# Kernel tuning notes

Measured on AMD Instinct MI355X. Metric: run time of the kernel, lower is better.

The kernel has to match this reference:

```python
import jax, jax.numpy as jnp
import numpy as np

# Grid derived from defaults: pc_range=(0,-40,-3,70.4,40,1), voxel=(0.2,0.2,4)
GX, GY = 352, 400          # round((70.4-0)/0.2), round((40-(-40))/0.2)
B, P = 4, 65536            # samples, points per sample
NSEG = B * GX * GY + 1     # dense pillar-id space + 1 sentinel for masked points
OUT_CH = 64
BN_EPS = 1e-3


def setup_inputs() -> dict:
    key = jax.random.key(0)
    k1, k2, k3 = jax.random.split(key, 3)
    xyz_min = jnp.array([0.0, -40.0, -3.0], jnp.float32)
    xyz_max = jnp.array([70.4, 40.0, 1.0], jnp.float32)
    xyz = jax.random.uniform(k1, (B, P, 3), jnp.float32, minval=xyz_min, maxval=xyz_max)
    rest = jax.random.normal(k2, (B, P, 4), jnp.float32)  # rcs, v_r, v_r_comp, time
    points = jnp.concatenate([xyz, rest], axis=-1)        # [B, P, 7]
    W = jax.random.normal(k3, (OUT_CH, 13), jnp.float32) * (1.0 / np.sqrt(13.0))
    gamma = jnp.ones((OUT_CH,), jnp.float32)
    beta = jnp.zeros((OUT_CH,), jnp.float32)
    return {"points": points, "W": W, "gamma": gamma, "beta": beta}


def reference(points, W, gamma, beta):
    Bn, Pn, _ = points.shape
    pts = points.reshape(Bn * Pn, 7)                      # [N, 7] (= torch points[:, 1:])
    dtype = pts.dtype
    voxel = jnp.array([0.2, 0.2, 4.0], dtype)
    pc_min = jnp.array([0.0, -40.0, -3.0], dtype)
    batch_idx = jnp.repeat(jnp.arange(Bn, dtype=jnp.int32), Pn)

    coords_f = (pts[:, :3] - pc_min) / voxel              # float voxel coords
    mask = ((coords_f[:, 0] >= 0) & (coords_f[:, 0] < GX)
            & (coords_f[:, 1] >= 0) & (coords_f[:, 1] < GY))
    coords = coords_f.astype(jnp.int32)                   # [N, 3] (cx, cy, cz)
    sentinel = Bn * GX * GY                               # trash segment for masked points
    lin = jnp.where(mask,
                    batch_idx * (GX * GY) + coords[:, 0] * GY + coords[:, 1],
                    sentinel)
    # torch.unique(..., return_inverse=True, dim=0) on (batch, cx, cy) rows ==
    # unique of the bijective linear id (same sorted order).
    unq, unq_inv = jnp.unique(lin, return_inverse=True, size=NSEG, fill_value=sentinel)

    cnt = jax.ops.segment_sum(jnp.ones((lin.shape[0], 1), dtype), unq_inv, num_segments=NSEG)
    mean_xyz = jax.ops.segment_sum(pts[:, :3], unq_inv, num_segments=NSEG) / jnp.maximum(cnt, 1.0)
    f_cluster = pts[:, :3] - mean_xyz[unq_inv]
    f_center = pts[:, :3] - (coords.astype(dtype) * voxel + voxel * 0.5 + pc_min)
    feats = jnp.concatenate([pts, f_cluster, f_center], axis=-1)   # [N, 13]

    # PFN layer (last_layer=True): Linear -> BN1d (training stats) -> ReLU
    x = feats @ W.T                                       # [N, 64]
    mu = x.mean(axis=0)
    var = x.var(axis=0)                                   # biased, as BN training
    x = jax.nn.relu((x - mu) * jax.lax.rsqrt(var + BN_EPS) * gamma + beta)

    fmax = jax.ops.segment_max(x, unq_inv, num_segments=NSEG)     # scatter_max
    x_max = fmax[unq_inv]                                 # gather back (PFN output)
    feat_max = jax.ops.segment_max(x_max, unq_inv, num_segments=NSEG)

    valid = (unq < sentinel)[:, None]                     # real pillars only
    feat_max = jnp.where(valid, feat_max, 0.0)            # padded/empty -> 0

    b = unq // (GX * GY)
    rem = unq % (GX * GY)
    cx = rem // GY
    cy = rem % GY
    coords_out = jnp.stack([b, cy, cx], axis=1).astype(jnp.int32)  # (batch, y, x)
    grid_size = jnp.array([GY, GX], jnp.int32)
    return feat_max, coords_out, grid_size
```

## Files before the change

### kernel.cpp

```cpp
#include <hip/hip_runtime.h>
#include <stdint.h>
#include <utility>

#define NPTS   262144
#define GXGY   140800
#define GYv    400
#define NSEG   563201
#define SENT   563200
#define NB_SCAN 275
#define PIL_BLOCKS 2048
#define MOMG_BLOCKS 512

constexpr size_t alignup(size_t x) { return (x + 255) & ~(size_t)255; }
constexpr size_t O_CNT  = 0;
constexpr size_t O_MOM  = alignup(O_CNT + (size_t)NSEG * 4);
constexpr size_t ZERO_BYTES = alignup(O_MOM + 104 * 4);
constexpr size_t O_PPTR = ZERO_BYTES;
constexpr size_t O_ROWI = alignup(O_PPTR + (size_t)NSEG * 4);
constexpr size_t O_FEAT = alignup(O_ROWI + (size_t)NPTS * 16);
constexpr size_t O_MEAN = alignup(O_FEAT + (size_t)NPTS * 32);
constexpr size_t O_BSO  = alignup(O_MEAN + (size_t)NPTS * 12);
constexpr size_t O_BSC  = alignup(O_BSO + NB_SCAN * 4);
constexpr size_t O_KP   = alignup(O_BSC + NB_SCAN * 4);
constexpr size_t O_WF   = alignup(O_KP + 256);
constexpr size_t O_SH   = alignup(O_WF + 832 * 4);

__device__ __forceinline__ int point_lin(float x, float y, int b, bool& mask) {
  float cxf = x / 0.2f;
  float cyf = (y + 40.0f) / 0.2f;
  int cx = (int)cxf, cy = (int)cyf;
  mask = (cxf >= 0.0f) && (cxf < 352.0f) && (cyf >= 0.0f) && (cyf < 400.0f);
  return mask ? (b * GXGY + cx * GYv + cy) : SENT;
}

__global__ __launch_bounds__(256) void k_count(const float* __restrict__ pts,
                                               unsigned int* __restrict__ cnt) {
  int i = blockIdx.x * 256 + threadIdx.x;
  if (i >= NPTS) return;
  const float* p = pts + (size_t)i * 7;
  float x = p[0], y = p[1];
  bool m;
  int lin = point_lin(x, y, i >> 16, m);
  atomicAdd(&cnt[lin], 1u);
}

__global__ __launch_bounds__(256) void k_scan1(const unsigned int* __restrict__ cnt,
                                               unsigned int* __restrict__ bso,
                                               unsigned int* __restrict__ bsc) {
  int t = threadIdx.x;
  int base = blockIdx.x * 2048 + t * 8;
  const uint4* c4 = (const uint4*)(cnt + base);
  uint4 a = c4[0], b = c4[1];
  unsigned so = (a.x > 0) + (a.y > 0) + (a.z > 0) + (a.w > 0) +
                (b.x > 0) + (b.y > 0) + (b.z > 0) + (b.w > 0);
  unsigned sc = a.x + a.y + a.z + a.w + b.x + b.y + b.z + b.w;
  for (int m = 1; m < 64; m <<= 1) { so += __shfl_xor(so, m); sc += __shfl_xor(sc, m); }
  __shared__ unsigned wo[4], wc[4];
  if ((t & 63) == 0) { wo[t >> 6] = so; wc[t >> 6] = sc; }
  __syncthreads();
  if (t == 0) {
    bso[blockIdx.x] = wo[0] + wo[1] + wo[2] + wo[3];
    bsc[blockIdx.x] = wc[0] + wc[1] + wc[2] + wc[3];
  }
}

__global__ __launch_bounds__(256) void k_scan3(const unsigned int* __restrict__ cnt,
                                               const unsigned int* __restrict__ bso,
                                               const unsigned int* __restrict__ bsc,
                                               uint4* __restrict__ rowinfo,
                                               unsigned int* __restrict__ pptr,
                                               unsigned int* __restrict__ kp) {
  int t = threadIdx.x;
  unsigned vo_m = 0, vc_m = 0, vo_a = 0;
  for (int e = t; e < NB_SCAN; e += 256) {
    unsigned o = bso[e], c = bsc[e];
    vo_a += o;
    if (e < (int)blockIdx.x) { vo_m += o; vc_m += c; }
  }
  for (int m = 1; m < 64; m <<= 1) {
    vo_m += __shfl_xor(vo_m, m);
    vc_m += __shfl_xor(vc_m, m);
    vo_a += __shfl_xor(vo_a, m);
  }
  __shared__ unsigned s0[4], s1[4], s2[4];
  int wv = t >> 6;
  if ((t & 63) == 0) { s0[wv] = vo_m; s1[wv] = vc_m; s2[wv] = vo_a; }
  __syncthreads();
  unsigned boo = s0[0] + s0[1] + s0[2] + s0[3];
  unsigned boc = s1[0] + s1[1] + s1[2] + s1[3];
  unsigned tot = s2[0] + s2[1] + s2[2] + s2[3];
  if (blockIdx.x == 0 && t == 0) *kp = tot;

  int base = blockIdx.x * 2048 + t * 8;
  const uint4* q = (const uint4*)(cnt + base);
  uint4 a = q[0], b = q[1];
  unsigned c[8] = {a.x, a.y, a.z, a.w, b.x, b.y, b.z, b.w};
  unsigned po[8], pc[8];
  unsigned so = 0, sc = 0;
#pragma unroll
  for (int k = 0; k < 8; k++) {
    po[k] = so; pc[k] = sc;
    so += (c[k] > 0); sc += c[k];
  }
  __shared__ unsigned sdo[256], sdc[256];
  __syncthreads();
  sdo[t] = so; sdc[t] = sc;
  __syncthreads();
  for (int off = 1; off < 256; off <<= 1) {
    unsigned ao = (t >= off) ? sdo[t - off] : 0u;
    unsigned ac = (t >= off) ? sdc[t - off] : 0u;
    __syncthreads();
    sdo[t] += ao; sdc[t] += ac;
    __syncthreads();
  }
  unsigned eo = sdo[t] - so + boo;
  unsigned ec = sdc[t] - sc + boc;
#pragma unroll
  for (int k = 0; k < 8; k++) {
    if (c[k] > 0) {
      unsigned r = eo + po[k];
      unsigned start = ec + pc[k];
      rowinfo[r] = make_uint4((unsigned)(base + k), start, c[k], 0u);
      pptr[base + k] = start;
    }
  }
}

__global__ __launch_bounds__(256) void k_sortfeat(const float* __restrict__ pts,
                                                  unsigned int* __restrict__ pptr,
                                                  float* __restrict__ feat) {
  int i = blockIdx.x * 256 + threadIdx.x;
  if (i >= NPTS) return;
  const float* p = pts + (size_t)i * 7;
  float x = p[0], y = p[1], z = p[2];
  bool m;
  int lin = point_lin(x, y, i >> 16, m);
  if (lin == SENT) return;
  unsigned pos = atomicAdd(&pptr[lin], 1u);
  float4* fb = (float4*)(feat + (size_t)pos * 8);
  fb[0] = make_float4(x, y, z, p[3]);
  fb[1] = make_float4(p[4], p[5], p[6], 0.0f);
}

constexpr int tri_j(int t) { int j = 0; while (t >= 13 - j) { t -= 13 - j; j++; } return j; }
constexpr int tri_k(int t) { int j = 0; while (t >= 13 - j) { t -= 13 - j; j++; } return j + t; }

template<int G, size_t U>
__device__ __forceinline__ void accum_one(const float (&f)[13], float (&acc)[52]) {
  constexpr int E = G * 52 + (int)U;
  if constexpr (E < 13) {
    acc[U] += f[E];
  } else {
    constexpr int J = tri_j(E - 13);
    constexpr int K = tri_k(E - 13);
    acc[U] += f[J] * f[K];
  }
}
template<int G, size_t... Us>
__device__ __forceinline__ void accum_all(const float (&f)[13], float (&acc)[52],
                                          std::index_sequence<Us...>) {
  (accum_one<G, Us>(f, acc), ...);
}

template<int G>
__device__ __forceinline__ void momrank_body(const uint4* __restrict__ rowinfo,
                                             const float* __restrict__ feat,
                                             float* __restrict__ meanr,
                                             float* __restrict__ mom,
                                             unsigned kp) {
  float acc[52];
#pragma unroll
  for (int u = 0; u < 52; u++) acc[u] = 0.f;
  const unsigned stride = MOMG_BLOCKS * 256;
  for (unsigned r = (blockIdx.x >> 1) * 256 + threadIdx.x; r < kp; r += stride) {
    uint4 ri = rowinfo[r];
    unsigned start = ri.y, n = ri.z;
    const float4* fp = (const float4*)(feat + (size_t)start * 8);
    float sx = 0.f, sy = 0.f, sz = 0.f;
    for (unsigned p = 0; p < n; p++) { float4 A = fp[2 * p]; sx += A.x; sy += A.y; sz += A.z; }
    float inv = 1.0f / fmaxf((float)n, 1.0f);
    float mx = sx * inv, my = sy * inv, mz = sz * inv;
    if (G == 0) {
      meanr[(size_t)r * 3 + 0] = mx;
      meanr[(size_t)r * 3 + 1] = my;
      meanr[(size_t)r * 3 + 2] = mz;
    }
    for (unsigned p = 0; p < n; p++) {
      float4 A = fp[2 * p], Bq = fp[2 * p + 1];
      float x = A.x, y = A.y, z = A.z;
      int cx = (int)(x / 0.2f);
      int cy = (int)((y + 40.0f) / 0.2f);
      int cz = (int)((z + 3.0f) / 4.0f);
      float f[13] = {x, y, z, A.w, Bq.x, Bq.y, Bq.z,
                     x - mx, y - my, z - mz,
                     x - ((float)cx * 0.2f + 0.1f + 0.0f),
                     y - ((float)cy * 0.2f + 0.1f - 40.0f),
                     z - ((float)cz * 4.0f + 2.0f - 3.0f)};
      accum_all<G>(f, acc, std::make_index_sequence<52>{});
    }
  }
  __shared__ float red[4][52];
  int wv = threadIdx.x >> 6, lane = threadIdx.x & 63;
#pragma unroll
  for (int u = 0; u < 52; u++) {
    float v = acc[u];
    v += __shfl_xor(v, 1);  v += __shfl_xor(v, 2);  v += __shfl_xor(v, 4);
    v += __shfl_xor(v, 8);  v += __shfl_xor(v, 16); v += __shfl_xor(v, 32);
    if (lane == 0) red[wv][u] = v;
  }
  __syncthreads();
  if (threadIdx.x < 52) {
    int u = threadIdx.x;
    atomicAdd(&mom[G * 52 + u], red[0][u] + red[1][u] + red[2][u] + red[3][u]);
  }
}

__global__ __launch_bounds__(256, 2) void k_momrank(const uint4* __restrict__ rowinfo,
                                                    const float* __restrict__ feat,
                                                    float* __restrict__ meanr,
                                                    float* __restrict__ mom,
                                                    const unsigned int* __restrict__ kpp) {
  unsigned kp = *kpp;
  if ((blockIdx.x & 1) == 0) momrank_body<0>(rowinfo, feat, meanr, mom, kp);
  else                       momrank_body<1>(rowinfo, feat, meanr, mom, kp);
}

__global__ void k_bnfinal(const float* __restrict__ W,
                          const float* __restrict__ g,
                          const float* __restrict__ bta,
                          const float* __restrict__ mom,
                          float* __restrict__ wf,
                          float* __restrict__ sh) {
  int c = threadIdx.x;
  float w[13];
#pragma unroll
  for (int j = 0; j < 13; j++) w[j] = W[c * 13 + j];
  const float invN = 1.0f / (float)NPTS;
  float mu = 0.f;
#pragma unroll
  for (int j = 0; j < 13; j++) mu += w[j] * (mom[j] * invN);
  float e2 = 0.f;
  int mi = 13;
#pragma unroll
  for (int j = 0; j < 13; j++) {
#pragma unroll
    for (int k = j; k < 13; k++) {
      float coef = (j == k) ? 1.0f : 2.0f;
      e2 += coef * w[j] * w[k] * mom[mi];
      mi++;
    }
  }
  e2 *= invN;
  float var = e2 - mu * mu;
  float rsig = 1.0f / sqrtf(var + 1e-3f);
  float sc = g[c] * rsig;
#pragma unroll
  for (int j = 0; j < 13; j++) wf[c * 13 + j] = w[j] * sc;
  sh[c] = bta[c] - mu * sc;
}

__global__ __launch_bounds__(256) void k_pillar(const float* __restrict__ wf,
                                                const float* __restrict__ sh,
                                                const uint4* __restrict__ rowinfo,
                                                const unsigned int* __restrict__ kp_p,
                                                const float* __restrict__ feat,
                                                const float* __restrict__ meanr,
                                                float* __restrict__ out) {
  int tid = threadIdx.x;
  int lane = tid & 15;
  int ch0 = lane * 4;
  float wr[52];
  float shv[4], wx[4], wy[4], wz[4];
#pragma unroll
  for (int c4 = 0; c4 < 4; c4++) {
    shv[c4] = sh[ch0 + c4];
#pragma unroll
    for (int j = 0; j < 13; j++) wr[c4 * 13 + j] = wf[(ch0 + c4) * 13 + j];
    wx[c4] = wr[c4 * 13 + 0] + wr[c4 * 13 + 7] + wr[c4 * 13 + 10];
    wy[c4] = wr[c4 * 13 + 1] + wr[c4 * 13 + 8] + wr[c4 * 13 + 11];
    wz[c4] = wr[c4 * 13 + 2] + wr[c4 * 13 + 9];
  }
  unsigned kp = *kp_p;

  const int NGRP = PIL_BLOCKS * 16;
  for (int r = blockIdx.x * 16 + (tid >> 4); r < NSEG; r += NGRP) {
    float m0 = -3.4e38f, m1 = -3.4e38f, m2 = -3.4e38f, m3 = -3.4e38f;
    int b = 4, cy = 0, cx = 0;
    if ((unsigned)r < kp) {
      uint4 ri = rowinfo[r];
      unsigned id = ri.x, start = ri.y, n = ri.z;
      b = id / GXGY;
      unsigned rem = id - (unsigned)b * GXGY;
      cx = rem / GYv;
      cy = rem - cx * GYv;
      float gx = (float)cx * 0.2f + 0.1f;
      float gy = (float)cy * 0.2f + 0.1f - 40.0f;
      float mx = meanr[(size_t)r * 3 + 0];
      float my = meanr[(size_t)r * 3 + 1];
      float mz = meanr[(size_t)r * 3 + 2];
      float s0_[4];
#pragma unroll
      for (int c4 = 0; c4 < 4; c4++) {
        s0_[c4] = shv[c4] - wr[c4 * 13 + 7] * mx - wr[c4 * 13 + 8] * my
                          - wr[c4 * 13 + 9] * mz - wr[c4 * 13 + 10] * gx
                          - wr[c4 * 13 + 11] * gy;
      }
      const float4* fb = (const float4*)(feat + (size_t)start * 8);
      for (unsigned p = 0; p < n; p++) {
        float4 A = fb[0], Bq = fb[1];
        fb += 2;
        int cz = (int)((A.z + 3.0f) / 4.0f);
        float fz = A.z - ((float)cz * 4.0f + 2.0f - 3.0f);
        float d0, d1, d2, d3;
#define DOT(dst, c4)                                                          \
        dst = s0_[c4];                                                        \
        dst += wx[c4] * A.x;            dst += wy[c4] * A.y;                  \
        dst += wz[c4] * A.z;            dst += wr[c4 * 13 + 3] * A.w;         \
        dst += wr[c4 * 13 + 4] * Bq.x;  dst += wr[c4 * 13 + 5] * Bq.y;        \
        dst += wr[c4 * 13 + 6] * Bq.z;  dst += wr[c4 * 13 + 12] * fz;
        DOT(d0, 0) DOT(d1, 1) DOT(d2, 2) DOT(d3, 3)
#undef DOT
        m0 = fmaxf(m0, d0); m1 = fmaxf(m1, d1);
        m2 = fmaxf(m2, d2); m3 = fmaxf(m3, d3);
      }
    }
    float4 v = make_float4(fmaxf(m0, 0.f), fmaxf(m1, 0.f),
                           fmaxf(m2, 0.f), fmaxf(m3, 0.f));
    *(float4*)(out + (size_t)r * 64 + lane * 4) = v;
    if (lane == 0) {
      float* cc = out + (size_t)NSEG * 64 + (size_t)r * 3;
      cc[0] = (float)b;
      cc[1] = (float)cy;
      cc[2] = (float)cx;
    }
  }
  if (blockIdx.x == 0 && tid == 0) {
    float* g2 = out + (size_t)NSEG * 67;
    g2[0] = 400.0f;
    g2[1] = 352.0f;
  }
}

extern "C" void kernel_launch(void* const* d_in, const int* in_sizes, int n_in,
                              void* d_out, int out_size, void* d_ws, size_t ws_size,
                              hipStream_t stream) {
  const float* pts = (const float*)d_in[0];
  const float* W   = (const float*)d_in[1];
  const float* g   = (const float*)d_in[2];
  const float* bta = (const float*)d_in[3];
  float* out = (float*)d_out;
  char* ws = (char*)d_ws;

  unsigned int* cnt  = (unsigned int*)(ws + O_CNT);
  float*        mom  = (float*)(ws + O_MOM);
  unsigned int* pptr = (unsigned int*)(ws + O_PPTR);
  uint4*        rowi = (uint4*)(ws + O_ROWI);
  float*        feat = (float*)(ws + O_FEAT);
  float*        mnr  = (float*)(ws + O_MEAN);
  unsigned int* bso  = (unsigned int*)(ws + O_BSO);
  unsigned int* bsc  = (unsigned int*)(ws + O_BSC);
  unsigned int* kp   = (unsigned int*)(ws + O_KP);
  float*        wf   = (float*)(ws + O_WF);
  float*        sh   = (float*)(ws + O_SH);
  (void)in_sizes; (void)n_in; (void)out_size; (void)ws_size;

  hipMemsetAsync(ws, 0, ZERO_BYTES, stream);

  k_count   <<<NPTS / 256, 256, 0, stream>>>(pts, cnt);
  k_scan1   <<<NB_SCAN, 256, 0, stream>>>(cnt, bso, bsc);
  k_scan3   <<<NB_SCAN, 256, 0, stream>>>(cnt, bso, bsc, rowi, pptr, kp);
  k_sortfeat<<<NPTS / 256, 256, 0, stream>>>(pts, pptr, feat);
  k_momrank <<<2 * MOMG_BLOCKS, 256, 0, stream>>>(rowi, feat, mnr, mom, kp);
  k_bnfinal <<<1, 64, 0, stream>>>(W, g, bta, mom, wf, sh);
  k_pillar  <<<PIL_BLOCKS, 256, 0, stream>>>(wf, sh, rowi, kp, feat, mnr, out);
}
```

Measured before the change: 256.0 us.

## Decompose BN moments into point-wise terms plus per-pillar mean corrections

The 13x13 second-moment accumulation is split algebraically. Moments of the 10 features that do not depend on the pillar mean are accumulated per point inside the count kernel. A much smaller set of per-pillar correction terms involving the cluster mean is computed in a new kernel, which also finalises the BN scale and shift in its last block through a done counter, removing the separate bnfinal launch. The pillar kernel recomputes the mean itself instead of reading a stored mean array. This cuts the heavy per-point 52-wide accumulation, but it adds an extra pass over each pillar's points in k_pillar and relies on a last-block pattern with atomics, which can change the float summation order.

```diff
diff --git a/kernel.cpp b/kernel.cpp
--- a/kernel.cpp
+++ b/kernel.cpp
@@ -9,17 +9,18 @@
 #define SENT   563200
 #define NB_SCAN 275
 #define PIL_BLOCKS 2048
-#define MOMG_BLOCKS 512
+#define CNT_BLOCKS 512
+#define PC_BLOCKS  512
 
 constexpr size_t alignup(size_t x) { return (x + 255) & ~(size_t)255; }
 constexpr size_t O_CNT  = 0;
 constexpr size_t O_MOM  = alignup(O_CNT + (size_t)NSEG * 4);
-constexpr size_t ZERO_BYTES = alignup(O_MOM + 104 * 4);
+constexpr size_t O_DONE = alignup(O_MOM + 104 * 4);
+constexpr size_t ZERO_BYTES = alignup(O_DONE + 256);
 constexpr size_t O_PPTR = ZERO_BYTES;
 constexpr size_t O_ROWI = alignup(O_PPTR + (size_t)NSEG * 4);
 constexpr size_t O_FEAT = alignup(O_ROWI + (size_t)NPTS * 16);
-constexpr size_t O_MEAN = alignup(O_FEAT + (size_t)NPTS * 32);
-constexpr size_t O_BSO  = alignup(O_MEAN + (size_t)NPTS * 12);
+constexpr size_t O_BSO  = alignup(O_FEAT + (size_t)NPTS * 32);
 constexpr size_t O_BSC  = alignup(O_BSO + NB_SCAN * 4);
 constexpr size_t O_KP   = alignup(O_BSC + NB_SCAN * 4);
 constexpr size_t O_WF   = alignup(O_KP + 256);
@@ -34,14 +35,63 @@
 }
 
 __global__ __launch_bounds__(256) void k_count(const float* __restrict__ pts,
-                                               unsigned int* __restrict__ cnt) {
-  int i = blockIdx.x * 256 + threadIdx.x;
-  if (i >= NPTS) return;
-  const float* p = pts + (size_t)i * 7;
-  float x = p[0], y = p[1];
-  bool m;
-  int lin = point_lin(x, y, i >> 16, m);
-  atomicAdd(&cnt[lin], 1u);
+                                               unsigned int* __restrict__ cnt,
+                                               float* __restrict__ mom) {
+  int tid = threadIdx.x;
+  float acc[65];
+#pragma unroll
+  for (int u = 0; u < 65; u++) acc[u] = 0.f;
+
+  for (int rep = 0; rep < 2; rep++) {
+    int i = rep * (CNT_BLOCKS * 256) + blockIdx.x * 256 + tid;
+    const float* p = pts + (size_t)i * 7;
+    float x = p[0], y = p[1], z = p[2];
+    float w3 = p[3], w4 = p[4], w5 = p[5], w6 = p[6];
+    bool m;
+    int lin = point_lin(x, y, i >> 16, m);
+    atomicAdd(&cnt[lin], 1u);
+    int cx = (int)(x / 0.2f);
+    int cy = (int)((y + 40.0f) / 0.2f);
+    int cz = (int)((z + 3.0f) / 4.0f);
+    float g[10] = {x, y, z, w3, w4, w5, w6,
+                   x - ((float)cx * 0.2f + 0.1f + 0.0f),
+                   y - ((float)cy * 0.2f + 0.1f - 40.0f),
+                   z - ((float)cz * 4.0f + 2.0f - 3.0f)};
+#pragma unroll
+    for (int q = 0; q < 10; q++) acc[q] += g[q];
+    int idx = 10;
+#pragma unroll
+    for (int pp = 0; pp < 10; pp++)
+#pragma unroll
+      for (int q = pp; q < 10; q++) { acc[idx] += g[pp] * g[q]; idx++; }
+  }
+
+  __shared__ float red[4][65];
+  int wv = tid >> 6, lane = tid & 63;
+#pragma unroll
+  for (int u = 0; u < 65; u++) {
+    float v = acc[u];
+    v += __shfl_xor(v, 1);  v += __shfl_xor(v, 2);  v += __shfl_xor(v, 4);
+    v += __shfl_xor(v, 8);  v += __shfl_xor(v, 16); v += __shfl_xor(v, 32);
+    if (lane == 0) red[wv][u] = v;
+  }
+  __syncthreads();
+  int t = tid;
+  if (t < 104 && !(t >= 7 && t <= 9)) {
+    int rix;
+    if (t < 13) {
+      rix = (t < 7) ? t : t - 3;
+    } else {
+      int u2 = t - 13, j = 0;
+      while (u2 >= 13 - j) { u2 -= 13 - j; j++; }
+      int k = j + u2;
+      int a = (j < 7) ? j : (j < 10 ? j - 7 : j - 3);
+      int b = (k < 7) ? k : (k < 10 ? k - 7 : k - 3);
+      int lo = a < b ? a : b, hi = a < b ? b : a;
+      rix = 10 + lo * (21 - lo) / 2 + (hi - lo);
+    }
+    atomicAdd(&mom[t], red[0][rix] + red[1][rix] + red[2][rix] + red[3][rix]);
+  }
 }
 
 __global__ __launch_bounds__(256) void k_scan1(const unsigned int* __restrict__ cnt,
@@ -142,121 +192,139 @@
   fb[1] = make_float4(p[4], p[5], p[6], 0.0f);
 }
 
-constexpr int tri_j(int t) { int j = 0; while (t >= 13 - j) { t -= 13 - j; j++; } return j; }
-constexpr int tri_k(int t) { int j = 0; while (t >= 13 - j) { t -= 13 - j; j++; } return j + t; }
-
-template<int G, size_t U>
-__device__ __forceinline__ void accum_one(const float (&f)[13], float (&acc)[52]) {
-  constexpr int E = G * 52 + (int)U;
-  if constexpr (E < 13) {
-    acc[U] += f[E];
-  } else {
-    constexpr int J = tri_j(E - 13);
-    constexpr int K = tri_k(E - 13);
-    acc[U] += f[J] * f[K];
-  }
-}
-template<int G, size_t... Us>
-__device__ __forceinline__ void accum_all(const float (&f)[13], float (&acc)[52],
-                                          std::index_sequence<Us...>) {
-  (accum_one<G, Us>(f, acc), ...);
-}
-
-template<int G>
-__device__ __forceinline__ void momrank_body(const uint4* __restrict__ rowinfo,
-                                             const float* __restrict__ feat,
-                                             float* __restrict__ meanr,
-                                             float* __restrict__ mom,
-                                             unsigned kp) {
-  float acc[52];
-#pragma unroll
-  for (int u = 0; u < 52; u++) acc[u] = 0.f;
-  const unsigned stride = MOMG_BLOCKS * 256;
-  for (unsigned r = (blockIdx.x >> 1) * 256 + threadIdx.x; r < kp; r += stride) {
+__global__ __launch_bounds__(256) void k_pilcorr(const uint4* __restrict__ rowinfo,
+                                                 const float* __restrict__ feat,
+                                                 const unsigned int* __restrict__ kpp,
+                                                 float* __restrict__ mom,
+                                                 unsigned int* __restrict__ done,
+                                                 const float* __restrict__ W,
+                                                 const float* __restrict__ g,
+                                                 const float* __restrict__ bta,
+                                                 float* __restrict__ wf,
+                                                 float* __restrict__ sh) {
+  int tid = threadIdx.x;
+  unsigned kp = *kpp;
+  float cS1[3] = {0.f, 0.f, 0.f};
+  float cAH[30], cUU[6];
+#pragma unroll
+  for (int u = 0; u < 30; u++) cAH[u] = 0.f;
+#pragma unroll
+  for (int u = 0; u < 6; u++) cUU[u] = 0.f;
+
+  for (unsigned r = blockIdx.x * 256 + tid; r < kp; r += PC_BLOCKS * 256) {
     uint4 ri = rowinfo[r];
     unsigned start = ri.y, n = ri.z;
     const float4* fp = (const float4*)(feat + (size_t)start * 8);
-    float sx = 0.f, sy = 0.f, sz = 0.f;
-    for (unsigned p = 0; p < n; p++) { float4 A = fp[2 * p]; sx += A.x; sy += A.y; sz += A.z; }
-    float inv = 1.0f / fmaxf((float)n, 1.0f);
-    float mx = sx * inv, my = sy * inv, mz = sz * inv;
-    if (G == 0) {
-      meanr[(size_t)r * 3 + 0] = mx;
-      meanr[(size_t)r * 3 + 1] = my;
-      meanr[(size_t)r * 3 + 2] = mz;
-    }
+    float S[10];
+#pragma unroll
+    for (int u = 0; u < 10; u++) S[u] = 0.f;
     for (unsigned p = 0; p < n; p++) {
       float4 A = fp[2 * p], Bq = fp[2 * p + 1];
       float x = A.x, y = A.y, z = A.z;
       int cx = (int)(x / 0.2f);
       int cy = (int)((y + 40.0f) / 0.2f);
       int cz = (int)((z + 3.0f) / 4.0f);
-      float f[13] = {x, y, z, A.w, Bq.x, Bq.y, Bq.z,
-                     x - mx, y - my, z - mz,
-                     x - ((float)cx * 0.2f + 0.1f + 0.0f),
-                     y - ((float)cy * 0.2f + 0.1f - 40.0f),
-                     z - ((float)cz * 4.0f + 2.0f - 3.0f)};
-      accum_all<G>(f, acc, std::make_index_sequence<52>{});
-    }
-  }
-  __shared__ float red[4][52];
-  int wv = threadIdx.x >> 6, lane = threadIdx.x & 63;
-#pragma unroll
-  for (int u = 0; u < 52; u++) {
-    float v = acc[u];
+      S[0] += x; S[1] += y; S[2] += z; S[3] += A.w;
+      S[4] += Bq.x; S[5] += Bq.y; S[6] += Bq.z;
+      S[7] += x - ((float)cx * 0.2f + 0.1f + 0.0f);
+      S[8] += y - ((float)cy * 0.2f + 0.1f - 40.0f);
+      S[9] += z - ((float)cz * 4.0f + 2.0f - 3.0f);
+    }
+    float fn = (float)n;
+    float mm[3] = {S[0] / fn, S[1] / fn, S[2] / fn};
+    cS1[0] += S[0] - fn * mm[0];
+    cS1[1] += S[1] - fn * mm[1];
+    cS1[2] += S[2] - fn * mm[2];
+#pragma unroll
+    for (int a = 0; a < 3; a++)
+#pragma unroll
+      for (int h = 0; h < 10; h++) cAH[a * 10 + h] += mm[a] * S[h];
+    int e = 0;
+#pragma unroll
+    for (int a = 0; a < 3; a++)
+#pragma unroll
+      for (int b = a; b < 3; b++) { cUU[e] += mm[a] * S[b]; e++; }
+  }
+
+  float vals[39];
+#pragma unroll
+  for (int u = 0; u < 3; u++)  vals[u] = cS1[u];
+#pragma unroll
+  for (int u = 0; u < 30; u++) vals[3 + u] = cAH[u];
+#pragma unroll
+  for (int u = 0; u < 6; u++)  vals[33 + u] = cUU[u];
+
+  __shared__ float red[4][39];
+  int wv = tid >> 6, lane = tid & 63;
+#pragma unroll
+  for (int u = 0; u < 39; u++) {
+    float v = vals[u];
     v += __shfl_xor(v, 1);  v += __shfl_xor(v, 2);  v += __shfl_xor(v, 4);
     v += __shfl_xor(v, 8);  v += __shfl_xor(v, 16); v += __shfl_xor(v, 32);
     if (lane == 0) red[wv][u] = v;
   }
   __syncthreads();
-  if (threadIdx.x < 52) {
-    int u = threadIdx.x;
-    atomicAdd(&mom[G * 52 + u], red[0][u] + red[1][u] + red[2][u] + red[3][u]);
-  }
-}
-
-__global__ __launch_bounds__(256, 2) void k_momrank(const uint4* __restrict__ rowinfo,
-                                                    const float* __restrict__ feat,
-                                                    float* __restrict__ meanr,
-                                                    float* __restrict__ mom,
-                                                    const unsigned int* __restrict__ kpp) {
-  unsigned kp = *kpp;
-  if ((blockIdx.x & 1) == 0) momrank_body<0>(rowinfo, feat, meanr, mom, kp);
-  else                       momrank_body<1>(rowinfo, feat, meanr, mom, kp);
-}
-
-__global__ void k_bnfinal(const float* __restrict__ W,
-                          const float* __restrict__ g,
-                          const float* __restrict__ bta,
-                          const float* __restrict__ mom,
-                          float* __restrict__ wf,
-                          float* __restrict__ sh) {
-  int c = threadIdx.x;
-  float w[13];
-#pragma unroll
-  for (int j = 0; j < 13; j++) w[j] = W[c * 13 + j];
-  const float invN = 1.0f / (float)NPTS;
-  float mu = 0.f;
-#pragma unroll
-  for (int j = 0; j < 13; j++) mu += w[j] * (mom[j] * invN);
-  float e2 = 0.f;
-  int mi = 13;
-#pragma unroll
-  for (int j = 0; j < 13; j++) {
-#pragma unroll
-    for (int k = j; k < 13; k++) {
-      float coef = (j == k) ? 1.0f : 2.0f;
-      e2 += coef * w[j] * w[k] * mom[mi];
-      mi++;
-    }
-  }
-  e2 *= invN;
-  float var = e2 - mu * mu;
-  float rsig = 1.0f / sqrtf(var + 1e-3f);
-  float sc = g[c] * rsig;
-#pragma unroll
-  for (int j = 0; j < 13; j++) wf[c * 13 + j] = w[j] * sc;
-  sh[c] = bta[c] - mu * sc;
+  if (tid < 39) {
+    float v = red[0][tid] + red[1][tid] + red[2][tid] + red[3][tid];
+    int slot; float sign;
+    if (tid < 3) {
+      slot = 7 + tid; sign = 1.f;
+    } else if (tid < 33) {
+      int a = (tid - 3) / 10, h = (tid - 3) % 10;
+      int hf = (h < 7) ? h : h + 3;
+      int j = hf < 7 + a ? hf : 7 + a;
+      int k = hf < 7 + a ? 7 + a : hf;
+      slot = 13 + j * (27 - j) / 2 + (k - j);
+      sign = -1.f;
+    } else {
+      int e = tid - 33;
+      int a = (e < 3) ? 0 : (e < 5 ? 1 : 2);
+      int b = (e < 3) ? e : (e < 5 ? e - 2 : 2);
+      int j = 7 + a, k = 7 + b;
+      slot = 13 + j * (27 - j) / 2 + (k - j);
+      sign = -1.f;
+    }
+    atomicAdd(&mom[slot], sign * v);
+  }
+
+  __threadfence();
+  __syncthreads();
+  __shared__ unsigned lastf;
+  if (tid == 0) lastf = (atomicAdd(done, 1u) == PC_BLOCKS - 1);
+  __syncthreads();
+  if (lastf) {
+    __shared__ float smom[104];
+    for (int u = tid; u < 104; u += 256) smom[u] = atomicAdd(&mom[u], 0.0f);
+    __syncthreads();
+    if (tid < 64) {
+      int c = tid;
+      float w[13];
+#pragma unroll
+      for (int j = 0; j < 13; j++) w[j] = W[c * 13 + j];
+      const float invN = 1.0f / (float)NPTS;
+      float mu = 0.f;
+#pragma unroll
+      for (int j = 0; j < 13; j++) mu += w[j] * (smom[j] * invN);
+      float e2 = 0.f;
+      int mi = 13;
+#pragma unroll
+      for (int j = 0; j < 13; j++) {
+#pragma unroll
+        for (int k = j; k < 13; k++) {
+          float coef = (j == k) ? 1.0f : 2.0f;
+          e2 += coef * w[j] * w[k] * smom[mi];
+          mi++;
+        }
+      }
+      e2 *= invN;
+      float var = e2 - mu * mu;
+      float rsig = 1.0f / sqrtf(var + 1e-3f);
+      float sc = g[c] * rsig;
+#pragma unroll
+      for (int j = 0; j < 13; j++) wf[c * 13 + j] = w[j] * sc;
+      sh[c] = bta[c] - mu * sc;
+    }
+  }
 }
 
 __global__ __launch_bounds__(256) void k_pillar(const float* __restrict__ wf,
@@ -264,7 +332,6 @@
                                                 const uint4* __restrict__ rowinfo,
                                                 const unsigned int* __restrict__ kp_p,
                                                 const float* __restrict__ feat,
-                                                const float* __restrict__ meanr,
                                                 float* __restrict__ out) {
   int tid = threadIdx.x;
   int lane = tid & 15;
@@ -295,9 +362,14 @@
       cy = rem - cx * GYv;
       float gx = (float)cx * 0.2f + 0.1f;
       float gy = (float)cy * 0.2f + 0.1f - 40.0f;
-      float mx = meanr[(size_t)r * 3 + 0];
-      float my = meanr[(size_t)r * 3 + 1];
-      float mz = meanr[(size_t)r * 3 + 2];
+      const float4* fb0 = (const float4*)(feat + (size_t)start * 8);
+      float sx = 0.f, sy = 0.f, sz = 0.f;
+      for (unsigned p = 0; p < n; p++) {
+        float4 A = fb0[2 * p];
+        sx += A.x; sy += A.y; sz += A.z;
+      }
+      float cm = (float)n;
+      float mx = sx / cm, my = sy / cm, mz = sz / cm;
       float s0_[4];
 #pragma unroll
       for (int c4 = 0; c4 < 4; c4++) {
@@ -305,7 +377,7 @@
                           - wr[c4 * 13 + 9] * mz - wr[c4 * 13 + 10] * gx
                           - wr[c4 * 13 + 11] * gy;
       }
-      const float4* fb = (const float4*)(feat + (size_t)start * 8);
+      const float4* fb = fb0;
       for (unsigned p = 0; p < n; p++) {
         float4 A = fb[0], Bq = fb[1];
         fb += 2;
@@ -353,10 +425,10 @@
 
   unsigned int* cnt  = (unsigned int*)(ws + O_CNT);
   float*        mom  = (float*)(ws + O_MOM);
+  unsigned int* done = (unsigned int*)(ws + O_DONE);
   unsigned int* pptr = (unsigned int*)(ws + O_PPTR);
   uint4*        rowi = (uint4*)(ws + O_ROWI);
   float*        feat = (float*)(ws + O_FEAT);
-  float*        mnr  = (float*)(ws + O_MEAN);
   unsigned int* bso  = (unsigned int*)(ws + O_BSO);
   unsigned int* bsc  = (unsigned int*)(ws + O_BSC);
   unsigned int* kp   = (unsigned int*)(ws + O_KP);
@@ -366,11 +438,10 @@
 
   hipMemsetAsync(ws, 0, ZERO_BYTES, stream);
 
-  k_count   <<<NPTS / 256, 256, 0, stream>>>(pts, cnt);
+  k_count   <<<CNT_BLOCKS, 256, 0, stream>>>(pts, cnt, mom);
   k_scan1   <<<NB_SCAN, 256, 0, stream>>>(cnt, bso, bsc);
   k_scan3   <<<NB_SCAN, 256, 0, stream>>>(cnt, bso, bsc, rowi, pptr, kp);
   k_sortfeat<<<NPTS / 256, 256, 0, stream>>>(pts, pptr, feat);
-  k_momrank <<<2 * MOMG_BLOCKS, 256, 0, stream>>>(rowi, feat, mnr, mom, kp);
-  k_bnfinal <<<1, 64, 0, stream>>>(W, g, bta, mom, wf, sh);
-  k_pillar  <<<PIL_BLOCKS, 256, 0, stream>>>(wf, sh, rowi, kp, feat, mnr, out);
-}
+  k_pilcorr <<<PC_BLOCKS, 256, 0, stream>>>(rowi, feat, kp, mom, done, W, g, bta, wf, sh);
+  k_pillar  <<<PIL_BLOCKS, 256, 0, stream>>>(wf, sh, rowi, kp, feat, out);
+}
```

After: 276.7 us. 8.1% more time.
